# Performance work log

Hardware: AMD Instinct MI355X
Metric: run time of the kernel (lower is better)

The kernel has to match this reference:

```python
import jax, jax.numpy as jnp
import numpy as np

BIG = 1e10  # large finite value standing in for +inf in masked mins (grad-safe)


def setup_inputs() -> dict:
    key = jax.random.key(0)
    k1, k2, k3 = jax.random.split(key, 3)
    B, C, N = 16, 3, 4096
    x = jax.random.normal(k1, (B, C, N), dtype=jnp.float32)
    y = jax.random.normal(k2, (B, C, N), dtype=jnp.float32)
    mask = jax.random.randint(k3, (B, N), 0, 2, dtype=jnp.int32)
    return {"x": x, "y": y, "mask": mask}


def reference(x, y, mask):
    # x, y: (B, 3, N); mask: (B, N) with 1 = valid point
    xt = jnp.swapaxes(x, 1, 2)  # (B, N, 3)
    yt = jnp.swapaxes(y, 1, 2)  # (B, N, 3)
    xx = jnp.sum(xt * xt, axis=-1)  # (B, N)
    yy = jnp.sum(yt * yt, axis=-1)  # (B, N)
    # squared pairwise distances, P[b, n, m] = ||x_bn - y_bm||^2
    P = xx[:, :, None] + yy[:, None, :] - 2.0 * jnp.einsum("bnd,bmd->bnm", xt, yt)

    valid = mask.astype(bool)                 # (B, N)
    mf = mask.astype(P.dtype)                 # (B, N)
    cnt = jnp.sum(mf, axis=1)                 # (B,) number of valid points per batch

    # direction 1: for each y-point m, min over valid x-rows n; mean over valid m
    mins1 = jnp.min(jnp.where(valid[:, :, None], P, BIG), axis=1)  # (B, N)
    means1 = jnp.sum(mins1 * mf, axis=1) / cnt                      # (B,)

    # direction 2: for each x-point m, min over valid y-cols n; mean over valid m
    mins2 = jnp.min(jnp.where(valid[:, None, :], P, BIG), axis=2)  # (B, N)
    means2 = jnp.sum(mins2 * mf, axis=1) / cnt                      # (B,)

    return jnp.mean(means1) + jnp.mean(means2)
```

## Files before the change

### kernel.cpp

```cpp
#include <hip/hip_runtime.h>

typedef short bf16x8 __attribute__((ext_vector_type(8)));
typedef float f32x16 __attribute__((ext_vector_type(16)));

#define BIG_F 1e10f
constexpr int B = 16;
constexpr int N = 4096;
constexpr int ROWS = 128;
constexpr int COLS = 512;
constexpr int NRB = N / ROWS;
constexpr int NCB = N / COLS;

__device__ __forceinline__ void split(float v, unsigned& h, unsigned& l) {
    unsigned hb = __float_as_uint(v) & 0xFFFF0000u;
    h = hb >> 16;
    float r = v - __uint_as_float(hb);
    l = __float_as_uint(r) >> 16;
}

__device__ __forceinline__ float min3f(float a, float b, float c) {
    return fminf(fminf(a, b), c);
}

__device__ __forceinline__ float vmin16(f32x16 C) {
    float u0 = min3f(C[0], C[1], C[2]);
    float u1 = min3f(C[3], C[4], C[5]);
    float u2 = min3f(C[6], C[7], C[8]);
    float u3 = min3f(C[9], C[10], C[11]);
    float u4 = min3f(C[12], C[13], C[14]);
    return min3f(min3f(u0, u1, u2), fminf(u3, u4), C[15]);
}

__device__ __forceinline__ float4 min4(float4 a, float4 b) {
    return make_float4(fminf(a.x, b.x), fminf(a.y, b.y),
                       fminf(a.z, b.z), fminf(a.w, b.w));
}

#define DPP_MIN(v, ctrl)                                                      \
    v = fminf(v, __int_as_float(__builtin_amdgcn_update_dpp(                  \
            __float_as_int(v), __float_as_int(v), (ctrl), 0xF, 0xF, false)))

__global__ __launch_bounds__(256, 4) void chamfer_mfma(
    const float* __restrict__ x, const float* __restrict__ y,
    const int* __restrict__ mask,
    float* __restrict__ rowpart,
    float* __restrict__ colpart,
    float* __restrict__ out)
{
    const int rb = blockIdx.x & 31;
    const int cb = blockIdx.x >> 5;
    const int b  = blockIdx.y;
    const int t  = threadIdx.x;

    __shared__ __align__(16) unsigned short Bpack[2][COLS][8];
    __shared__ float colbuf[8][COLS];

    if (blockIdx.x == 0 && b == 0 && t == 0) out[0] = 0.0f;

    const float* xb = x + (size_t)b * 3 * N;
    const float* yb = y + (size_t)b * 3 * N;
    const int*   mb = mask + b * N;

#pragma unroll
    for (int i = 0; i < 2; ++i) {
        int c = t + i * 256;
        int m = cb * COLS + c;
        float y0 = yb[m], y1 = yb[N + m], y2 = yb[2 * N + m];
        float madd = mb[m] ? 0.0f : BIG_F;
        float yy = fmaf(y2, y2, fmaf(y1, y1, y0 * y0)) + madd;
        unsigned h0, l0, h1, l1, h2, l2, qh, ql;
        split(y0, h0, l0);
        split(y1, h1, l1);
        split(y2, h2, l2);
        split(yy, qh, ql);
        unsigned u0 = h0 | (h1 << 16);
        unsigned u1 = h2 | (l0 << 16);
        unsigned u2 = l1 | (l2 << 16);
        uint4 w0 = { u0, u1, u2, u0 };
        uint4 w1 = { u1, u2, 0x3F803F80u, qh | (ql << 16) };
        *(uint4*)&Bpack[0][c][0] = w0;
        *(uint4*)&Bpack[1][c][0] = w1;
    }

    const int w    = t >> 6;
    const int L    = t & 63;
    const int half = L >> 5;
    const int lc   = L & 31;

    bf16x8 afr;
    {
        int n = rb * ROWS + w * 32 + lc;
        float x0 = xb[n], x1 = xb[N + n], x2 = xb[2 * N + n];
        float madd = mb[n] ? 0.0f : BIG_F;
        float xx = fmaf(x2, x2, fmaf(x1, x1, x0 * x0)) + madd;
        unsigned h0, l0, h1, l1, h2, l2, xh, xl;
        split(-2.0f * x0, h0, l0);
        split(-2.0f * x1, h1, l1);
        split(-2.0f * x2, h2, l2);
        split(xx, xh, xl);
        uint4 wa;
        wa.x = half ? (l2 | (l0 << 16)) : (h0 | (h1 << 16));
        wa.y = half ? (l1 | (l2 << 16)) : (h2 | (h0 << 16));
        wa.z = half ? (xh | (xl << 16)) : (h1 | (h2 << 16));
        wa.w = half ? 0x3F803F80u       : (l0 | (l1 << 16));
        afr = *(bf16x8*)&wa;
    }

    __syncthreads();

    const unsigned short* Bb = &Bpack[half][lc][0];

    float rm[16];
#pragma unroll
    for (int r = 0; r < 16; ++r) rm[r] = 1e30f;

    const f32x16 z16 = {0.f,0.f,0.f,0.f,0.f,0.f,0.f,0.f,
                        0.f,0.f,0.f,0.f,0.f,0.f,0.f,0.f};

    bf16x8 nb0 = *(const bf16x8*)(Bb);
    bf16x8 nb1 = *(const bf16x8*)(Bb + 256);

#pragma unroll 1
    for (int p = 0; p < 8; ++p) {
        bf16x8 bf0 = nb0, bf1 = nb1;
        int pn = (p + 1) & 7;
        nb0 = *(const bf16x8*)(Bb + pn * 512);
        nb1 = *(const bf16x8*)(Bb + pn * 512 + 256);

        f32x16 C0 = __builtin_amdgcn_mfma_f32_32x32x16_bf16(afr, bf0, z16, 0, 0, 0);
        f32x16 C1 = __builtin_amdgcn_mfma_f32_32x32x16_bf16(afr, bf1, z16, 0, 0, 0);
#pragma unroll
        for (int r = 0; r < 16; ++r) rm[r] = min3f(rm[r], C0[r], C1[r]);
        colbuf[w * 2 + half][p * 64 + lc]      = vmin16(C0);
        colbuf[w * 2 + half][p * 64 + 32 + lc] = vmin16(C1);
    }

#pragma unroll
    for (int r = 0; r < 16; ++r) {
        DPP_MIN(rm[r], 0xB1);
        DPP_MIN(rm[r], 0x4E);
        DPP_MIN(rm[r], 0x124);
        DPP_MIN(rm[r], 0x128);
    }
    if ((lc & 15) == 0) {
        int sset = lc >> 4;
        float* rp = rowpart + (((size_t)(b * NCB + cb)) * 2 + sset) * N
                  + rb * ROWS + w * 32 + half * 4;
        *(float4*)(rp +  0) = make_float4(rm[0],  rm[1],  rm[2],  rm[3]);
        *(float4*)(rp +  8) = make_float4(rm[4],  rm[5],  rm[6],  rm[7]);
        *(float4*)(rp + 16) = make_float4(rm[8],  rm[9],  rm[10], rm[11]);
        *(float4*)(rp + 24) = make_float4(rm[12], rm[13], rm[14], rm[15]);
    }

    __syncthreads();
    if (t < 128) {
        const float4* cb4 = (const float4*)&colbuf[0][0];
        float4 v = cb4[t];
#pragma unroll
        for (int s = 1; s < 8; ++s) v = min4(v, cb4[s * 128 + t]);
        *(float4*)(colpart + ((size_t)b * NRB + rb) * N + cb * COLS + t * 4) = v;
    }
}

__global__ __launch_bounds__(256) void finalize_kernel(
    const int* __restrict__ mask,
    const float* __restrict__ rowpart, const float* __restrict__ colpart,
    float* __restrict__ out)
{
    const int b = blockIdx.x & 15;
    const int q = blockIdx.x >> 4;
    const int t = threadIdx.x;
    const int* mrow = mask + b * N;

    int cnt = 0;
    for (int i = t; i < N / 4; i += 256) {
        int4 mk = ((const int4*)mrow)[i];
        cnt += mk.x + mk.y + mk.z + mk.w;
    }

    const int p0 = q * 1024 + t * 4;
    const float* cp = colpart + (size_t)b * NRB * N + p0;
    const float* rp = rowpart + (size_t)b * NCB * 2 * N + p0;

    float4 mn = *(const float4*)cp;
    float4 rn = *(const float4*)rp;
#pragma unroll 8
    for (int pb = 1; pb < NRB; ++pb) {
        mn = min4(mn, *(const float4*)(cp + (size_t)pb * N));
        if (pb < NCB * 2)
            rn = min4(rn, *(const float4*)(rp + (size_t)pb * N));
    }
    int4 mk = *(const int4*)(mrow + p0);
    float s = (mk.x ? (mn.x + rn.x) : 0.f) + (mk.y ? (mn.y + rn.y) : 0.f)
            + (mk.z ? (mn.z + rn.z) : 0.f) + (mk.w ? (mn.w + rn.w) : 0.f);

    for (int off = 32; off > 0; off >>= 1) {
        s   += __shfl_down(s, off);
        cnt += __shfl_down(cnt, off);
    }
    __shared__ float rs[4];
    __shared__ int   rc[4];
    const int wv = t >> 6;
    if ((t & 63) == 0) { rs[wv] = s; rc[wv] = cnt; }
    __syncthreads();
    if (t == 0) {
        float S = rs[0] + rs[1] + rs[2] + rs[3];
        float C = (float)(rc[0] + rc[1] + rc[2] + rc[3]);
        atomicAdd(out, (S / C) * (1.0f / 16.0f));
    }
}

extern "C" void kernel_launch(void* const* d_in, const int* in_sizes, int n_in,
                              void* d_out, int out_size, void* d_ws, size_t ws_size,
                              hipStream_t stream) {
    const float* x    = (const float*)d_in[0];
    const float* y    = (const float*)d_in[1];
    const int*   mask = (const int*)d_in[2];

    float* rowpart = (float*)d_ws;
    float* colpart = rowpart + (size_t)B * NCB * 2 * N;

    chamfer_mfma<<<dim3(NRB * NCB, B), 256, 0, stream>>>(
        x, y, mask, rowpart, colpart, (float*)d_out);
    finalize_kernel<<<dim3(64), 256, 0, stream>>>(
        mask, rowpart, colpart, (float*)d_out);
}
```

Baseline: 91.89 us.

## Process four row tiles per block, reusing packed Y tile and accumulating column minima

Each block now loops over four 128-row jobs, reusing the packed Y columns staged in LDS, instead of handling one row tile. The grid shrinks from 4096 to 1024 blocks. Column minima are accumulated across jobs in LDS, so the colpart buffer and the finalize reduction drop from 32 to 8 partials per point. This cuts redundant Y loading, packing and global partial traffic, but gives less parallelism per launch and adds a read-modify-write on LDS for each job.

```diff
diff --git a/kernel.cpp b/kernel.cpp
--- a/kernel.cpp
+++ b/kernel.cpp
@@ -6,10 +6,11 @@
 #define BIG_F 1e10f
 constexpr int B = 16;
 constexpr int N = 4096;
-constexpr int ROWS = 128;
 constexpr int COLS = 512;
-constexpr int NRB = N / ROWS;
 constexpr int NCB = N / COLS;
+constexpr int JOBS = 4;
+constexpr int SUBROWS = 128 * JOBS;
+constexpr int NSB = N / SUBROWS;
 
 __device__ __forceinline__ void split(float v, unsigned& h, unsigned& l) {
     unsigned hb = __float_as_uint(v) & 0xFFFF0000u;
@@ -47,15 +48,16 @@
     float* __restrict__ colpart,
     float* __restrict__ out)
 {
-    const int rb = blockIdx.x & 31;
-    const int cb = blockIdx.x >> 5;
-    const int b  = blockIdx.y;
-    const int t  = threadIdx.x;
+    const int blk = blockIdx.x;
+    const int b   = blk >> 6;
+    const int cb  = (blk >> 3) & 7;
+    const int sub = blk & 7;
+    const int t   = threadIdx.x;
 
     __shared__ __align__(16) unsigned short Bpack[2][COLS][8];
     __shared__ float colbuf[8][COLS];
 
-    if (blockIdx.x == 0 && b == 0 && t == 0) out[0] = 0.0f;
+    if (blk == 0 && t == 0) out[0] = 0.0f;
 
     const float* xb = x + (size_t)b * 3 * N;
     const float* yb = y + (size_t)b * 3 * N;
@@ -87,69 +89,79 @@
     const int half = L >> 5;
     const int lc   = L & 31;
 
-    bf16x8 afr;
-    {
-        int n = rb * ROWS + w * 32 + lc;
-        float x0 = xb[n], x1 = xb[N + n], x2 = xb[2 * N + n];
-        float madd = mb[n] ? 0.0f : BIG_F;
-        float xx = fmaf(x2, x2, fmaf(x1, x1, x0 * x0)) + madd;
-        unsigned h0, l0, h1, l1, h2, l2, xh, xl;
-        split(-2.0f * x0, h0, l0);
-        split(-2.0f * x1, h1, l1);
-        split(-2.0f * x2, h2, l2);
-        split(xx, xh, xl);
-        uint4 wa;
-        wa.x = half ? (l2 | (l0 << 16)) : (h0 | (h1 << 16));
-        wa.y = half ? (l1 | (l2 << 16)) : (h2 | (h0 << 16));
-        wa.z = half ? (xh | (xl << 16)) : (h1 | (h2 << 16));
-        wa.w = half ? 0x3F803F80u       : (l0 | (l1 << 16));
-        afr = *(bf16x8*)&wa;
-    }
-
     __syncthreads();
 
     const unsigned short* Bb = &Bpack[half][lc][0];
-
-    float rm[16];
-#pragma unroll
-    for (int r = 0; r < 16; ++r) rm[r] = 1e30f;
+    float* cacc0 = &colbuf[w * 2 + half][lc];
 
     const f32x16 z16 = {0.f,0.f,0.f,0.f,0.f,0.f,0.f,0.f,
                         0.f,0.f,0.f,0.f,0.f,0.f,0.f,0.f};
 
-    bf16x8 nb0 = *(const bf16x8*)(Bb);
-    bf16x8 nb1 = *(const bf16x8*)(Bb + 256);
-
 #pragma unroll 1
-    for (int p = 0; p < 8; ++p) {
-        bf16x8 bf0 = nb0, bf1 = nb1;
-        int pn = (p + 1) & 7;
-        nb0 = *(const bf16x8*)(Bb + pn * 512);
-        nb1 = *(const bf16x8*)(Bb + pn * 512 + 256);
-
-        f32x16 C0 = __builtin_amdgcn_mfma_f32_32x32x16_bf16(afr, bf0, z16, 0, 0, 0);
-        f32x16 C1 = __builtin_amdgcn_mfma_f32_32x32x16_bf16(afr, bf1, z16, 0, 0, 0);
-#pragma unroll
-        for (int r = 0; r < 16; ++r) rm[r] = min3f(rm[r], C0[r], C1[r]);
-        colbuf[w * 2 + half][p * 64 + lc]      = vmin16(C0);
-        colbuf[w * 2 + half][p * 64 + 32 + lc] = vmin16(C1);
-    }
-
-#pragma unroll
-    for (int r = 0; r < 16; ++r) {
-        DPP_MIN(rm[r], 0xB1);
-        DPP_MIN(rm[r], 0x4E);
-        DPP_MIN(rm[r], 0x124);
-        DPP_MIN(rm[r], 0x128);
-    }
-    if ((lc & 15) == 0) {
-        int sset = lc >> 4;
-        float* rp = rowpart + (((size_t)(b * NCB + cb)) * 2 + sset) * N
-                  + rb * ROWS + w * 32 + half * 4;
-        *(float4*)(rp +  0) = make_float4(rm[0],  rm[1],  rm[2],  rm[3]);
-        *(float4*)(rp +  8) = make_float4(rm[4],  rm[5],  rm[6],  rm[7]);
-        *(float4*)(rp + 16) = make_float4(rm[8],  rm[9],  rm[10], rm[11]);
-        *(float4*)(rp + 24) = make_float4(rm[12], rm[13], rm[14], rm[15]);
+    for (int jj = 0; jj < JOBS; ++jj) {
+        bf16x8 afr;
+        {
+            int n = sub * SUBROWS + jj * 128 + w * 32 + lc;
+            float x0 = xb[n], x1 = xb[N + n], x2 = xb[2 * N + n];
+            float madd = mb[n] ? 0.0f : BIG_F;
+            float xx = fmaf(x2, x2, fmaf(x1, x1, x0 * x0)) + madd;
+            unsigned h0, l0, h1, l1, h2, l2, xh, xl;
+            split(-2.0f * x0, h0, l0);
+            split(-2.0f * x1, h1, l1);
+            split(-2.0f * x2, h2, l2);
+            split(xx, xh, xl);
+            uint4 wa;
+            wa.x = half ? (l2 | (l0 << 16)) : (h0 | (h1 << 16));
+            wa.y = half ? (l1 | (l2 << 16)) : (h2 | (h0 << 16));
+            wa.z = half ? (xh | (xl << 16)) : (h1 | (h2 << 16));
+            wa.w = half ? 0x3F803F80u       : (l0 | (l1 << 16));
+            afr = *(bf16x8*)&wa;
+        }
+
+        float rm[16];
+#pragma unroll
+        for (int r = 0; r < 16; ++r) rm[r] = 1e30f;
+
+        bf16x8 nb0 = *(const bf16x8*)(Bb);
+        bf16x8 nb1 = *(const bf16x8*)(Bb + 256);
+
+#pragma unroll 1
+        for (int p = 0; p < 8; ++p) {
+            bf16x8 bf0 = nb0, bf1 = nb1;
+            int pn = (p + 1) & 7;
+            nb0 = *(const bf16x8*)(Bb + pn * 512);
+            nb1 = *(const bf16x8*)(Bb + pn * 512 + 256);
+
+            f32x16 C0 = __builtin_amdgcn_mfma_f32_32x32x16_bf16(afr, bf0, z16, 0, 0, 0);
+            f32x16 C1 = __builtin_amdgcn_mfma_f32_32x32x16_bf16(afr, bf1, z16, 0, 0, 0);
+#pragma unroll
+            for (int r = 0; r < 16; ++r) rm[r] = min3f(rm[r], C0[r], C1[r]);
+            float v0 = vmin16(C0), v1 = vmin16(C1);
+            if (jj == 0) {
+                cacc0[p * 64]      = v0;
+                cacc0[p * 64 + 32] = v1;
+            } else {
+                cacc0[p * 64]      = fminf(cacc0[p * 64],      v0);
+                cacc0[p * 64 + 32] = fminf(cacc0[p * 64 + 32], v1);
+            }
+        }
+
+#pragma unroll
+        for (int r = 0; r < 16; ++r) {
+            DPP_MIN(rm[r], 0xB1);
+            DPP_MIN(rm[r], 0x4E);
+            DPP_MIN(rm[r], 0x124);
+            DPP_MIN(rm[r], 0x128);
+        }
+        if ((lc & 15) == 0) {
+            int sset = lc >> 4;
+            float* rp = rowpart + (((size_t)(b * NCB + cb)) * 2 + sset) * N
+                      + sub * SUBROWS + jj * 128 + w * 32 + half * 4;
+            *(float4*)(rp +  0) = make_float4(rm[0],  rm[1],  rm[2],  rm[3]);
+            *(float4*)(rp +  8) = make_float4(rm[4],  rm[5],  rm[6],  rm[7]);
+            *(float4*)(rp + 16) = make_float4(rm[8],  rm[9],  rm[10], rm[11]);
+            *(float4*)(rp + 24) = make_float4(rm[12], rm[13], rm[14], rm[15]);
+        }
     }
 
     __syncthreads();
@@ -158,7 +170,7 @@
         float4 v = cb4[t];
 #pragma unroll
         for (int s = 1; s < 8; ++s) v = min4(v, cb4[s * 128 + t]);
-        *(float4*)(colpart + ((size_t)b * NRB + rb) * N + cb * COLS + t * 4) = v;
+        *(float4*)(colpart + ((size_t)b * NSB + sub) * N + cb * COLS + t * 4) = v;
     }
 }
 
@@ -179,16 +191,16 @@
     }
 
     const int p0 = q * 1024 + t * 4;
-    const float* cp = colpart + (size_t)b * NRB * N + p0;
+    const float* cp = colpart + (size_t)b * NSB * N + p0;
     const float* rp = rowpart + (size_t)b * NCB * 2 * N + p0;
 
     float4 mn = *(const float4*)cp;
     float4 rn = *(const float4*)rp;
 #pragma unroll 8
-    for (int pb = 1; pb < NRB; ++pb) {
-        mn = min4(mn, *(const float4*)(cp + (size_t)pb * N));
-        if (pb < NCB * 2)
-            rn = min4(rn, *(const float4*)(rp + (size_t)pb * N));
+    for (int pb = 1; pb < NCB * 2; ++pb) {
+        rn = min4(rn, *(const float4*)(rp + (size_t)pb * N));
+        if (pb < NSB)
+            mn = min4(mn, *(const float4*)(cp + (size_t)pb * N));
     }
     int4 mk = *(const int4*)(mrow + p0);
     float s = (mk.x ? (mn.x + rn.x) : 0.f) + (mk.y ? (mn.y + rn.y) : 0.f)
@@ -220,7 +232,7 @@
     float* rowpart = (float*)d_ws;
     float* colpart = rowpart + (size_t)B * NCB * 2 * N;
 
-    chamfer_mfma<<<dim3(NRB * NCB, B), 256, 0, stream>>>(
+    chamfer_mfma<<<dim3(B * NCB * NSB), 256, 0, stream>>>(
         x, y, mask, rowpart, colpart, (float*)d_out);
     finalize_kernel<<<dim3(64), 256, 0, stream>>>(
         mask, rowpart, colpart, (float*)d_out);
```

Measured after the change: 86.91 us. 1.06x faster.
